# Optimization experiments

Measured on AMD Instinct MI355X. Metric: run time of the kernel, lower is better.

## Reference

```python
import jax, jax.numpy as jnp
import numpy as np

NUM_HEADS = 12


def get_rel_pos(q_size, k_size, rel_pos):
    # rel_pos: (2*max(q,k)-1, head_dim); sizes match table here so no resize.
    max_rel_dist = int(2 * max(q_size, k_size) - 1)
    if rel_pos.shape[0] != max_rel_dist:
        rel_pos = jax.image.resize(rel_pos, (max_rel_dist, rel_pos.shape[1]), method='linear')
    q_coords = jnp.arange(q_size)[:, None] * max(k_size / q_size, 1.0)
    k_coords = jnp.arange(k_size)[None, :] * max(q_size / k_size, 1.0)
    rel = (q_coords - k_coords + (k_size - 1) * max(q_size / k_size, 1.0)).astype(jnp.int32)
    return rel_pos[rel.reshape(-1)].reshape(q_size, k_size, -1)  # (q, k, head_dim)


def setup_inputs() -> dict:
    key = jax.random.key(0)
    ks = jax.random.split(key, 7)
    B, H, W, C = 8, 32, 32, 768
    head_dim = C // NUM_HEADS
    return {
        'x': jax.random.normal(ks[0], (B, H, W, C), jnp.float32),
        'w_qkv': jax.random.normal(ks[1], (C, 3 * C), jnp.float32) * 0.02,
        'b_qkv': jnp.zeros((3 * C,), jnp.float32),
        'rel_pos_h': jax.random.normal(ks[2], (2 * H - 1, head_dim), jnp.float32) * 0.02,
        'rel_pos_w': jax.random.normal(ks[3], (2 * W - 1, head_dim), jnp.float32) * 0.02,
        'w_proj': jax.random.normal(ks[4], (C, C), jnp.float32) * 0.02,
        'b_proj': jnp.zeros((C,), jnp.float32),
    }


def reference(x, w_qkv, b_qkv, rel_pos_h, rel_pos_w, w_proj, b_proj):
    B, H, W, C = x.shape
    heads = NUM_HEADS
    hd = C // heads
    S = H * W
    qkv = x @ w_qkv + b_qkv                                  # (B,H,W,3C)
    qkv = qkv.reshape(B, S, 3, heads, hd).transpose(2, 0, 3, 1, 4)
    qkv = qkv.reshape(3, B * heads, S, hd)
    q, k, v = qkv[0], qkv[1], qkv[2]
    attn = (q * hd ** -0.5) @ k.transpose(0, 2, 1)           # (B*heads, S, S)
    rh = get_rel_pos(H, H, rel_pos_h)                        # (H,H,hd)
    rw = get_rel_pos(W, W, rel_pos_w)                        # (W,W,hd)
    r_q = q.reshape(B * heads, H, W, hd)
    rel_h = jnp.einsum('bhwc,hkc->bhwk', r_q, rh)
    rel_w = jnp.einsum('bhwc,wkc->bhwk', r_q, rw)
    attn = (attn.reshape(B * heads, H, W, H, W)
            + rel_h[:, :, :, :, None]
            + rel_w[:, :, :, None, :]).reshape(B * heads, S, S)
    attn = jax.nn.softmax(attn, axis=-1)
    out = (attn @ v).reshape(B, heads, H, W, hd).transpose(0, 2, 3, 1, 4).reshape(B, H, W, C)
    return out @ w_proj + b_proj
```

## Files before the change

### kernel.cpp

```cpp
#include <hip/hip_runtime.h>
#include <hip/hip_bf16.h>

#define BATCH 8
#define SEQ   1024
#define CH    768
#define NH    12
#define HD    64
#define BH    96
#define N_QKV 2304

#define LOG2E 1.44269504088896f

typedef __attribute__((ext_vector_type(8))) short bfrag;
typedef __attribute__((ext_vector_type(4))) short short4v;
typedef __attribute__((ext_vector_type(4))) float ffrag;
typedef __attribute__((ext_vector_type(4))) int  intv4;
typedef __attribute__((ext_vector_type(2))) int  intv2;

__device__ __forceinline__ short f2bf(float x) {
    __hip_bfloat16 h = __float2bfloat16(x);
    return *reinterpret_cast<short*>(&h);
}
__device__ __forceinline__ float bf2f(short b) {
    __hip_bfloat16 h;
    *reinterpret_cast<short*>(&h) = b;
    return __bfloat162float(h);
}
__device__ __forceinline__ void split2(float x, short& hi, short& lo) {
    short h = f2bf(x);
    hi = h;
    lo = f2bf(x - bf2f(h));
}
__device__ __forceinline__ void async_copy16(void* lds, const void* g) {
    __builtin_amdgcn_global_load_lds(
        (const __attribute__((address_space(1))) void*)g,
        (__attribute__((address_space(3))) void*)lds, 16, 0, 0);
}
__device__ __forceinline__ void pinned_load16(intv4& dst, const void* p) {
    asm volatile("global_load_dwordx4 %0, %1, off"
                 : "=&v"(dst) : "v"((unsigned long long)p));
}

__global__ __launch_bounds__(256) void prep(
    const float* __restrict__ x,
    const float* __restrict__ w_qkv, const float* __restrict__ w_proj,
    short* __restrict__ Xh,
    short* __restrict__ WqhT,
    short* __restrict__ WphT, short* __restrict__ WplT)
{
    __shared__ float ts[32][33];
    const int tid = threadIdx.x;
    const int bid = blockIdx.x;

    if (bid < 512) {
        const int n4 = (BATCH * SEQ * CH) / 4;
        for (int i = bid * 256 + tid; i < n4; i += 512 * 256) {
            float4 f = ((const float4*)x)[i];
            short4v h;
            h[0] = f2bf(f.x); h[1] = f2bf(f.y); h[2] = f2bf(f.z); h[3] = f2bf(f.w);
            ((short4v*)Xh)[i] = h;
        }
        return;
    }
    if (bid < 2240) {
        int t = bid - 512;
        const int bx = t % 72, by = t / 72;
        const int r0 = by * 32, c0 = bx * 32;
        #pragma unroll
        for (int i = 0; i < 4; ++i) {
            int idx = tid + i * 256;
            int rr = idx >> 5, cc = idx & 31;
            ts[rr][cc] = w_qkv[(size_t)(r0 + rr) * N_QKV + c0 + cc];
        }
        __syncthreads();
        #pragma unroll
        for (int i = 0; i < 4; ++i) {
            int idx = tid + i * 256;
            int rr = idx >> 5, cc = idx & 31;
            WqhT[(size_t)(c0 + rr) * CH + r0 + cc] = f2bf(ts[cc][rr]);
        }
        return;
    }
    {
        int t = bid - 2240;
        const int bx = t % 24, by = t / 24;
        const int r0 = by * 32, c0 = bx * 32;
        #pragma unroll
        for (int i = 0; i < 4; ++i) {
            int idx = tid + i * 256;
            int rr = idx >> 5, cc = idx & 31;
            ts[rr][cc] = w_proj[(size_t)(r0 + rr) * CH + c0 + cc];
        }
        __syncthreads();
        #pragma unroll
        for (int i = 0; i < 4; ++i) {
            int idx = tid + i * 256;
            int rr = idx >> 5, cc = idx & 31;
            short h, l;
            split2(ts[cc][rr], h, l);
            WphT[(size_t)(c0 + rr) * CH + r0 + cc] = h;
            WplT[(size_t)(c0 + rr) * CH + r0 + cc] = l;
        }
    }
}

__device__ __forceinline__ void gemm_core1(
    short* lds,
    const short* __restrict__ Ah, const short* __restrict__ BhT,
    int m0, int n0, ffrag acc[4][4])
{
    const int tid = threadIdx.x;
    const int wave = tid >> 6, lane = tid & 63;
    const int quad = lane >> 4, l16 = lane & 15;
    const int wm = (wave & 1) * 64, wn = (wave >> 1) * 64;

    const int arr  = wave >> 1;
    const int half = wave & 1;
    const short* src = arr ? BhT : Ah;
    const int row0 = (arr ? n0 : m0) + half * 64;
    const size_t lane_off = (size_t)(lane >> 3) * CH + (size_t)((lane & 7) ^ (lane >> 3)) * 8;
    const short* sbase = src + (size_t)row0 * CH + lane_off;
    short* ldsw = lds + arr * 8192 + half * 4096;

    for (int c = 0; c < 12; ++c) {
        __syncthreads();
        #pragma unroll
        for (int i = 0; i < 8; ++i)
            async_copy16(ldsw + i * 512, sbase + (size_t)i * 8 * CH + c * 64);
        __syncthreads();

        #pragma unroll
        for (int kc = 0; kc < 2; ++kc) {
            bfrag ah[4], bh[4];
            const int xs = ((kc * 4 + quad) ^ (l16 & 7)) * 8;
            #pragma unroll
            for (int i = 0; i < 4; ++i) {
                ah[i] = *(const bfrag*)&lds[(wm + i * 16 + l16) * 64 + xs];
                bh[i] = *(const bfrag*)&lds[8192 + (wn + i * 16 + l16) * 64 + xs];
            }
            #pragma unroll
            for (int mi = 0; mi < 4; ++mi)
                #pragma unroll
                for (int ni = 0; ni < 4; ++ni)
                    acc[mi][ni] = __builtin_amdgcn_mfma_f32_16x16x32_bf16(ah[mi], bh[ni], acc[mi][ni], 0, 0, 0);
        }
    }
}

__device__ __forceinline__ void gemm_core3(
    short* lds,
    const short* __restrict__ Ah, const short* __restrict__ Al,
    const short* __restrict__ BhT, const short* __restrict__ BlT,
    int m0, int n0, ffrag acc[4][4])
{
    const int tid = threadIdx.x;
    const int wave = tid >> 6, lane = tid & 63;
    const int quad = lane >> 4, l16 = lane & 15;
    const int wm = (wave & 1) * 64, wn = (wave >> 1) * 64;

    const short* src;
    int row0;
    if (wave == 0)      { src = Ah;  row0 = m0; }
    else if (wave == 1) { src = Al;  row0 = m0; }
    else if (wave == 2) { src = BhT; row0 = n0; }
    else                { src = BlT; row0 = n0; }
    const size_t lane_off = (size_t)(lane >> 3) * CH + (size_t)((lane & 7) ^ (lane >> 3)) * 8;
    const short* sbase = src + (size_t)row0 * CH + lane_off;
    short* ldsw = lds + wave * 8192;

    for (int c = 0; c < 12; ++c) {
        __syncthreads();
        #pragma unroll
        for (int i = 0; i < 16; ++i)
            async_copy16(ldsw + i * 512, sbase + (size_t)i * 8 * CH + c * 64);
        __syncthreads();

        #pragma unroll
        for (int kc = 0; kc < 2; ++kc) {
            bfrag ah[4], al[4], bh[4], bl[4];
            const int xs = ((kc * 4 + quad) ^ (l16 & 7)) * 8;
            #pragma unroll
            for (int i = 0; i < 4; ++i) {
                int ra = (wm + i * 16 + l16) * 64 + xs;
                int rb = (wn + i * 16 + l16) * 64 + xs;
                ah[i] = *(const bfrag*)&lds[ra];
                al[i] = *(const bfrag*)&lds[8192 + ra];
                bh[i] = *(const bfrag*)&lds[16384 + rb];
                bl[i] = *(const bfrag*)&lds[24576 + rb];
            }
            #pragma unroll
            for (int mi = 0; mi < 4; ++mi)
                #pragma unroll
                for (int ni = 0; ni < 4; ++ni) {
                    acc[mi][ni] = __builtin_amdgcn_mfma_f32_16x16x32_bf16(ah[mi], bh[ni], acc[mi][ni], 0, 0, 0);
                    acc[mi][ni] = __builtin_amdgcn_mfma_f32_16x16x32_bf16(ah[mi], bl[ni], acc[mi][ni], 0, 0, 0);
                    acc[mi][ni] = __builtin_amdgcn_mfma_f32_16x16x32_bf16(al[mi], bh[ni], acc[mi][ni], 0, 0, 0);
                }
        }
    }
}

__global__ __launch_bounds__(256) void gemm_qkv_mfma(
    const short* __restrict__ Xh,
    const short* __restrict__ WhT,
    const float* __restrict__ bias,
    short* __restrict__ qh, short* __restrict__ kh, short* __restrict__ vT)
{
    __shared__ short lds[2 * 8192];
    const int id  = blockIdx.x;
    const int xcd = id & 7;
    const int per = id >> 3;
    const int mi_ = per & 7;
    const int ni_ = per >> 3;
    const int m0 = (xcd * 8 + mi_) * 128;
    const int n0 = ni_ * 128;
    const int which = n0 / CH;

    ffrag acc[4][4];
    #pragma unroll
    for (int i = 0; i < 4; ++i)
        #pragma unroll
        for (int j = 0; j < 4; ++j) acc[i][j] = (ffrag){0.f, 0.f, 0.f, 0.f};

    gemm_core1(lds, Xh, WhT, m0, n0, acc);

    const int tid = threadIdx.x;
    const int wave = tid >> 6, lane = tid & 63;
    const int quad = lane >> 4, l16 = lane & 15;
    const int wm = (wave & 1) * 64, wn = (wave >> 1) * 64;
    const int b = m0 >> 10;

    #pragma unroll
    for (int ni = 0; ni < 4; ++ni) {
        int n = n0 + wn + ni * 16 + l16;
        float bv = bias[n];
        int nin = n - which * CH;
        int head = nin >> 6, d = nin & 63;
        #pragma unroll
        for (int mi = 0; mi < 4; ++mi) {
            if (which == 2) {
                int s_base = (m0 & 1023) + wm + mi * 16 + quad * 4;
                short4v pk;
                #pragma unroll
                for (int r = 0; r < 4; ++r) pk[r] = f2bf(acc[mi][ni][r] + bv);
                *(short4v*)&vT[((size_t)(b * NH + head) * HD + d) * SEQ + s_base] = pk;
            } else {
                const float scale = (which == 0) ? 0.125f * LOG2E : 1.0f;
                short* dst = (which == 0) ? qh : kh;
                #pragma unroll
                for (int r = 0; r < 4; ++r) {
                    int m = m0 + wm + mi * 16 + quad * 4 + r;
                    int s = m & 1023;
                    dst[((size_t)(b * NH + head) * SEQ + s) * HD + d] =
                        f2bf((acc[mi][ni][r] + bv) * scale);
                }
            }
        }
    }
}

__global__ __launch_bounds__(256) void gemm_proj_mfma(
    const short* __restrict__ Ah, const short* __restrict__ Al,
    const short* __restrict__ WhT, const short* __restrict__ WlT,
    const float* __restrict__ bias, float* __restrict__ out)
{
    __shared__ short lds[4 * 8192];
    const int id  = blockIdx.x;
    const int xcd = id & 7;
    const int per = id >> 3;
    const int mi_ = per & 7;
    const int ni_ = per >> 3;
    const int m0 = (xcd * 8 + mi_) * 128;
    const int n0 = ni_ * 128;

    ffrag acc[4][4];
    #pragma unroll
    for (int i = 0; i < 4; ++i)
        #pragma unroll
        for (int j = 0; j < 4; ++j) acc[i][j] = (ffrag){0.f, 0.f, 0.f, 0.f};

    gemm_core3(lds, Ah, Al, WhT, WlT, m0, n0, acc);

    const int tid = threadIdx.x;
    const int wave = tid >> 6, lane = tid & 63;
    const int quad = lane >> 4, l16 = lane & 15;
    const int wm = (wave & 1) * 64, wn = (wave >> 1) * 64;

    #pragma unroll
    for (int ni = 0; ni < 4; ++ni) {
        int n = n0 + wn + ni * 16 + l16;
        float bv = bias[n];
        #pragma unroll
        for (int mi = 0; mi < 4; ++mi)
            #pragma unroll
            for (int r = 0; r < 4; ++r) {
                int m = m0 + wm + mi * 16 + quad * 4 + r;
                out[(size_t)m * CH + n] = acc[mi][ni][r] + bv;
            }
    }
}

__global__ __launch_bounds__(256, 3) void attn_kernel(
    const short* __restrict__ qh,
    const short* __restrict__ kh_g, const short* __restrict__ vT_g,
    const float* __restrict__ rph,
    const float* __restrict__ rpw,
    short* __restrict__ aoh, short* __restrict__ aol)
{
    const int fid   = blockIdx.x;
    const int xcd   = fid & 7;
    const int inner = fid >> 3;
    const int s0    = (inner & 7) * 128;
    const int bh    = xcd * 12 + (inner >> 3);

    const int tid  = threadIdx.x;
    const int wave = tid >> 6;
    const int lane = tid & 63;
    const int quad = lane >> 4;
    const int l16  = lane & 15;

    __shared__ short Kh[64 * 64];
    __shared__ short Vth[64 * 64];
    __shared__ short Th[128][68];
    __shared__ short Tw_Ps[128 * 68];

    const size_t bh_koff = (size_t)bh * SEQ * HD;
    const size_t bh_voff = (size_t)bh * HD * SEQ;
    const size_t klane = (size_t)(lane >> 3) * HD + (size_t)((lane & 7) ^ (lane >> 3)) * 8;

    const short* kbase = kh_g + bh_koff + klane;
    const int i0 = wave * 2;
    short* KhW0 = Kh + i0 * 512 + lane * 8;

    const short* vgbase = vT_g + bh_voff
        + (size_t)(wave * 16 + (lane >> 3)) * SEQ + (size_t)(lane & 7) * 8;

    int vwA[2], vwB[2];
    {
        const int m  = lane & 7;
        const int oA = ((m >> 2) << 2) + ((m & 1) << 1);
        const int hf = (m >> 1) & 1;
        #pragma unroll
        for (int jj = 0; jj < 2; ++jj) {
            int d = wave * 16 + jj * 8 + (lane >> 3);
            vwA[jj] = d * 64 + ((oA ^ (d & 7)) << 3) + hf * 4;
            vwB[jj] = d * 64 + (((oA + 1) ^ (d & 7)) << 3) + hf * 4;
        }
    }

    intv4 kA0, kA1, vA0, vA1, kB0, kB1, vB0, vB1;
    pinned_load16(kA0, kbase + (size_t)(i0 * 8) * HD);
    pinned_load16(kA1, kbase + (size_t)(i0 * 8 + 8) * HD);
    pinned_load16(vA0, vgbase);
    pinned_load16(vA1, vgbase + (size_t)8 * SEQ);

    bfrag qfh[2][2];
    #pragma unroll
    for (int g = 0; g < 2; ++g) {
        const size_t qrow = ((size_t)bh * SEQ + s0 + wave * 32 + g * 16 + l16) * HD;
        #pragma unroll
        for (int kc = 0; kc < 2; ++kc)
            qfh[g][kc] = *(const bfrag*)(qh + qrow + kc * 32 + quad * 8);
    }

    #pragma unroll
    for (int table = 0; table < 2; ++table) {
        const float* tbl = table ? rpw : rph;
        #pragma unroll
        for (int n0r = 0; n0r < 64; n0r += 16) {
            int r = n0r + l16;
            bfrag bfr[2];
            #pragma unroll
            for (int kc = 0; kc < 2; ++kc) {
                if (r < 63) {
                    const float* trow = tbl + (size_t)r * HD + kc * 32 + quad * 8;
                    float4 f0 = *(const float4*)(trow);
                    float4 f1 = *(const float4*)(trow + 4);
                    float xs[8] = {f0.x, f0.y, f0.z, f0.w, f1.x, f1.y, f1.z, f1.w};
                    #pragma unroll
                    for (int j = 0; j < 8; ++j) bfr[kc][j] = f2bf(xs[j]);
                } else {
                    #pragma unroll
                    for (int j = 0; j < 8; ++j) bfr[kc][j] = 0;
                }
            }
            #pragma unroll
            for (int g = 0; g < 2; ++g) {
                ffrag acc = {0.f, 0.f, 0.f, 0.f};
                acc = __builtin_amdgcn_mfma_f32_16x16x32_bf16(qfh[g][0], bfr[0], acc, 0, 0, 0);
                acc = __builtin_amdgcn_mfma_f32_16x16x32_bf16(qfh[g][1], bfr[1], acc, 0, 0, 0);
                int row = wave * 32 + g * 16 + quad * 4;
                #pragma unroll
                for (int reg = 0; reg < 4; ++reg) {
                    short v = f2bf(acc[reg] * 8.0f);
                    if (table) Tw_Ps[(row + reg) * 68 + n0r + l16] = v;
                    else       Th[row + reg][n0r + l16] = v;
                }
            }
        }
    }

    float tw_r[2][2][4];
    #pragma unroll
    for (int g = 0; g < 2; ++g) {
        int qloc = wave * 32 + g * 16 + l16;
        int wq = g * 16 + l16;
        #pragma unroll
        for (int p = 0; p < 2; ++p)
            #pragma unroll
            for (int reg = 0; reg < 4; ++reg)
                tw_r[g][p][reg] = bf2f(Tw_Ps[qloc * 68 + (wq - (p * 16 + quad * 4 + reg) + 31)]);
    }
    const int hq_w = (s0 >> 5) + wave;

    float l_part[2] = {0.f, 0.f};
    ffrag Ot[2][4];
    #pragma unroll
    for (int g = 0; g < 2; ++g)
        #pragma unroll
        for (int t = 0; t < 4; ++t) Ot[g][t] = (ffrag){0.f, 0.f, 0.f, 0.f};

    auto chunk = [&](int c, const intv4& ck0, const intv4& ck1,
                     const intv4& cv0, const intv4& cv1,
                     intv4& nk0, intv4& nk1, intv4& nv0, intv4& nv1) {
        __syncthreads();
        if (c < 15) {
            const int cn = c + 1;
            pinned_load16(nk0, kbase + (size_t)(cn * 64 + i0 * 8) * HD);
            pinned_load16(nk1, kbase + (size_t)(cn * 64 + i0 * 8 + 8) * HD);
            pinned_load16(nv0, vgbase + cn * 64);
            pinned_load16(nv1, vgbase + (size_t)8 * SEQ + cn * 64);
            asm volatile("s_waitcnt vmcnt(4)");
        } else {
            asm volatile("s_waitcnt vmcnt(0)");
        }
        __builtin_amdgcn_sched_barrier(0);
        *(intv4*)KhW0         = ck0;
        *(intv4*)(KhW0 + 512) = ck1;
        {
            intv2 lo0 = {cv0[0], cv0[1]}, hi0 = {cv0[2], cv0[3]};
            intv2 lo1 = {cv1[0], cv1[1]}, hi1 = {cv1[2], cv1[3]};
            *(intv2*)&Vth[vwA[0]] = lo0;
            *(intv2*)&Vth[vwB[0]] = hi0;
            *(intv2*)&Vth[vwA[1]] = lo1;
            *(intv2*)&Vth[vwB[1]] = hi1;
        }
        __syncthreads();

        float th_r[2][2];
        #pragma unroll
        for (int g = 0; g < 2; ++g) {
            int qloc = wave * 32 + g * 16 + l16;
            th_r[g][0] = bf2f(Th[qloc][hq_w - 2 * c + 31]);
            th_r[g][1] = bf2f(Th[qloc][hq_w - 2 * c - 1 + 31]);
        }

        #pragma unroll
        for (int ktp = 0; ktp < 2; ++ktp) {
            bfrag kbhE[2], kbhO[2];
            #pragma unroll
            for (int kc = 0; kc < 2; ++kc) {
                int xs = ((kc * 4 + quad) ^ (l16 & 7)) * 8;
                kbhE[kc] = *(const bfrag*)&Kh[((2 * ktp) * 16 + l16) * 64 + xs];
                kbhO[kc] = *(const bfrag*)&Kh[((2 * ktp + 1) * 16 + l16) * 64 + xs];
            }
            bfrag pf[2];
            #pragma unroll
            for (int g = 0; g < 2; ++g) {
                ffrag aE, aO;
                #pragma unroll
                for (int reg = 0; reg < 4; ++reg) {
                    aE[reg] = th_r[g][ktp] + tw_r[g][0][reg];
                    aO[reg] = th_r[g][ktp] + tw_r[g][1][reg];
                }
                __builtin_amdgcn_s_setprio(1);
                aE = __builtin_amdgcn_mfma_f32_16x16x32_bf16(kbhE[0], qfh[g][0], aE, 0, 0, 0);
                aE = __builtin_amdgcn_mfma_f32_16x16x32_bf16(kbhE[1], qfh[g][1], aE, 0, 0, 0);
                aO = __builtin_amdgcn_mfma_f32_16x16x32_bf16(kbhO[0], qfh[g][0], aO, 0, 0, 0);
                aO = __builtin_amdgcn_mfma_f32_16x16x32_bf16(kbhO[1], qfh[g][1], aO, 0, 0, 0);
                __builtin_amdgcn_s_setprio(0);
                #pragma unroll
                for (int reg = 0; reg < 4; ++reg) {
                    float pE = exp2f(aE[reg]);
                    float pO = exp2f(aO[reg]);
                    l_part[g] += pE + pO;
                    pf[g][reg]     = f2bf(pE);
                    pf[g][reg + 4] = f2bf(pO);
                }
            }
            #pragma unroll
            for (int t = 0; t < 4; ++t) {
                int d = t * 16 + l16;
                int xv = ((ktp * 4 + quad) ^ (l16 & 7)) * 8;
                bfrag vh = *(const bfrag*)&Vth[d * 64 + xv];
                __builtin_amdgcn_s_setprio(1);
                #pragma unroll
                for (int g = 0; g < 2; ++g)
                    Ot[g][t] = __builtin_amdgcn_mfma_f32_16x16x32_bf16(pf[g], vh, Ot[g][t], 0, 0, 0);
                __builtin_amdgcn_s_setprio(0);
            }
        }
    };

    for (int cc = 0; cc < 8; ++cc) {
        chunk(2 * cc,     kA0, kA1, vA0, vA1, kB0, kB1, vB0, vB1);
        chunk(2 * cc + 1, kB0, kB1, vB0, vB1, kA0, kA1, vA0, vA1);
    }

    {
        int b = bh / NH, head = bh % NH;
        #pragma unroll
        for (int g = 0; g < 2; ++g) {
            float r = l_part[g];
            r += __shfl_xor(r, 16, 64);
            r += __shfl_xor(r, 32, 64);
            float invl = 1.f / r;
            float inv[4];
            #pragma unroll
            for (int reg = 0; reg < 4; ++reg)
                inv[reg] = __shfl(invl, quad * 4 + reg, 16);
            #pragma unroll
            for (int t = 0; t < 4; ++t) {
                #pragma unroll
                for (int reg = 0; reg < 4; ++reg) {
                    int s_ = s0 + wave * 32 + g * 16 + quad * 4 + reg;
                    int d = t * 16 + l16;
                    size_t idx = ((size_t)(b * SEQ + s_)) * CH + head * HD + d;
                    short h, l;
                    split2(Ot[g][t][reg] * inv[reg], h, l);
                    aoh[idx] = h;
                    aol[idx] = l;
                }
            }
        }
    }
}

extern "C" void kernel_launch(void* const* d_in, const int* in_sizes, int n_in,
                              void* d_out, int out_size, void* d_ws, size_t ws_size,
                              hipStream_t stream) {
    const float* x       = (const float*)d_in[0];
    const float* w_qkv   = (const float*)d_in[1];
    const float* b_qkv   = (const float*)d_in[2];
    const float* rph     = (const float*)d_in[3];
    const float* rpw     = (const float*)d_in[4];
    const float* w_proj  = (const float*)d_in[5];
    const float* b_proj  = (const float*)d_in[6];
    float* out = (float*)d_out;

    const size_t NTOK = (size_t)BATCH * SEQ;
    const size_t XSZ  = NTOK * CH;
    const size_t WQSZ = (size_t)N_QKV * CH;
    const size_t WPSZ = (size_t)CH * CH;
    short* Xh   = (short*)d_ws;
    short* AoL  = Xh + XSZ;
    short* WqhT = AoL + XSZ;
    short* WphT = WqhT + WQSZ;
    short* WplT = WphT + WPSZ;
    short* qh = WplT + WPSZ;
    short* kh = qh + XSZ;
    short* vT = kh + XSZ;
    short* aoh = Xh;
    short* aol = AoL;

    prep<<<dim3(2816), 256, 0, stream>>>(x, w_qkv, w_proj,
                                         Xh, WqhT, WphT, WplT);
    gemm_qkv_mfma<<<dim3(1152), 256, 0, stream>>>(Xh, WqhT, b_qkv,
                                                  qh, kh, vT);
    attn_kernel<<<dim3(768), 256, 0, stream>>>(qh, kh, vT,
                                               rph, rpw, aoh, aol);
    gemm_proj_mfma<<<dim3(384), 256, 0, stream>>>(aoh, aol, WphT, WplT,
                                                  b_proj, out);
}
```

Before: 226.0 us.

## Double-buffer LDS in QKV and projection GEMM cores with K-chunk prefetch

Result: no change. 227.2 us (+0.6%).

```diff
diff --git a/kernel.cpp b/kernel.cpp
--- a/kernel.cpp
+++ b/kernel.cpp
@@ -118,32 +118,48 @@
     const int half = wave & 1;
     const short* src = arr ? BhT : Ah;
     const int row0 = (arr ? n0 : m0) + half * 64;
-    const size_t lane_off = (size_t)(lane >> 3) * CH + (size_t)((lane & 7) ^ (lane >> 3)) * 8;
+    const size_t lane_off = (size_t)(lane >> 2) * CH
+                          + (size_t)((lane & 3) ^ ((lane >> 3) & 3)) * 8;
     const short* sbase = src + (size_t)row0 * CH + lane_off;
-    short* ldsw = lds + arr * 8192 + half * 4096;
-
-    for (int c = 0; c < 12; ++c) {
-        __syncthreads();
-        #pragma unroll
-        for (int i = 0; i < 8; ++i)
-            async_copy16(ldsw + i * 512, sbase + (size_t)i * 8 * CH + c * 64);
-        __syncthreads();
-
-        #pragma unroll
-        for (int kc = 0; kc < 2; ++kc) {
-            bfrag ah[4], bh[4];
-            const int xs = ((kc * 4 + quad) ^ (l16 & 7)) * 8;
-            #pragma unroll
-            for (int i = 0; i < 4; ++i) {
-                ah[i] = *(const bfrag*)&lds[(wm + i * 16 + l16) * 64 + xs];
-                bh[i] = *(const bfrag*)&lds[8192 + (wn + i * 16 + l16) * 64 + xs];
-            }
-            #pragma unroll
-            for (int mi = 0; mi < 4; ++mi)
-                #pragma unroll
-                for (int ni = 0; ni < 4; ++ni)
-                    acc[mi][ni] = __builtin_amdgcn_mfma_f32_16x16x32_bf16(ah[mi], bh[ni], acc[mi][ni], 0, 0, 0);
-        }
+    short* wsec = lds + arr * 4096 + half * 2048;
+
+    const int xs = (quad ^ ((l16 >> 1) & 3)) * 8;
+
+    #pragma unroll
+    for (int i = 0; i < 4; ++i)
+        async_copy16(wsec + i * 512, sbase + (size_t)i * 16 * CH);
+
+    for (int c = 0; c < 24; ++c) {
+        const int cur = c & 1;
+        if (c < 23) {
+            short* w = wsec + (cur ^ 1) * 8192;
+            #pragma unroll
+            for (int i = 0; i < 4; ++i)
+                async_copy16(w + i * 512,
+                             sbase + (size_t)i * 16 * CH + (c + 1) * 32);
+            asm volatile("s_waitcnt vmcnt(4)");
+        } else {
+            asm volatile("s_waitcnt vmcnt(0)");
+        }
+        __builtin_amdgcn_s_barrier();
+        __builtin_amdgcn_sched_barrier(0);
+
+        const short* Ab = lds + cur * 8192;
+        const short* Bb = Ab + 4096;
+        bfrag ah[4], bh[4];
+        #pragma unroll
+        for (int i = 0; i < 4; ++i) {
+            ah[i] = *(const bfrag*)&Ab[(wm + i * 16 + l16) * 32 + xs];
+            bh[i] = *(const bfrag*)&Bb[(wn + i * 16 + l16) * 32 + xs];
+        }
+        #pragma unroll
+        for (int mi = 0; mi < 4; ++mi)
+            #pragma unroll
+            for (int ni = 0; ni < 4; ++ni)
+                acc[mi][ni] = __builtin_amdgcn_mfma_f32_16x16x32_bf16(
+                    ah[mi], bh[ni], acc[mi][ni], 0, 0, 0);
+
+        __builtin_amdgcn_s_barrier();
     }
 }
 
@@ -164,39 +180,53 @@
     else if (wave == 1) { src = Al;  row0 = m0; }
     else if (wave == 2) { src = BhT; row0 = n0; }
     else                { src = BlT; row0 = n0; }
-    const size_t lane_off = (size_t)(lane >> 3) * CH + (size_t)((lane & 7) ^ (lane >> 3)) * 8;
+    const size_t lane_off = (size_t)(lane >> 2) * CH
+                          + (size_t)((lane & 3) ^ ((lane >> 3) & 3)) * 8;
     const short* sbase = src + (size_t)row0 * CH + lane_off;
-    short* ldsw = lds + wave * 8192;
-
-    for (int c = 0; c < 12; ++c) {
-        __syncthreads();
-        #pragma unroll
-        for (int i = 0; i < 16; ++i)
-            async_copy16(ldsw + i * 512, sbase + (size_t)i * 8 * CH + c * 64);
-        __syncthreads();
-
-        #pragma unroll
-        for (int kc = 0; kc < 2; ++kc) {
-            bfrag ah[4], al[4], bh[4], bl[4];
-            const int xs = ((kc * 4 + quad) ^ (l16 & 7)) * 8;
-            #pragma unroll
-            for (int i = 0; i < 4; ++i) {
-                int ra = (wm + i * 16 + l16) * 64 + xs;
-                int rb = (wn + i * 16 + l16) * 64 + xs;
-                ah[i] = *(const bfrag*)&lds[ra];
-                al[i] = *(const bfrag*)&lds[8192 + ra];
-                bh[i] = *(const bfrag*)&lds[16384 + rb];
-                bl[i] = *(const bfrag*)&lds[24576 + rb];
-            }
-            #pragma unroll
-            for (int mi = 0; mi < 4; ++mi)
-                #pragma unroll
-                for (int ni = 0; ni < 4; ++ni) {
-                    acc[mi][ni] = __builtin_amdgcn_mfma_f32_16x16x32_bf16(ah[mi], bh[ni], acc[mi][ni], 0, 0, 0);
-                    acc[mi][ni] = __builtin_amdgcn_mfma_f32_16x16x32_bf16(ah[mi], bl[ni], acc[mi][ni], 0, 0, 0);
-                    acc[mi][ni] = __builtin_amdgcn_mfma_f32_16x16x32_bf16(al[mi], bh[ni], acc[mi][ni], 0, 0, 0);
-                }
-        }
+    short* wsec = lds + wave * 4096;
+
+    const int xs = (quad ^ ((l16 >> 1) & 3)) * 8;
+
+    #pragma unroll
+    for (int i = 0; i < 8; ++i)
+        async_copy16(wsec + i * 512, sbase + (size_t)i * 16 * CH);
+
+    for (int c = 0; c < 24; ++c) {
+        const int cur = c & 1;
+        if (c < 23) {
+            short* w = wsec + (cur ^ 1) * 16384;
+            #pragma unroll
+            for (int i = 0; i < 8; ++i)
+                async_copy16(w + i * 512,
+                             sbase + (size_t)i * 16 * CH + (c + 1) * 32);
+            asm volatile("s_waitcnt vmcnt(8)");
+        } else {
+            asm volatile("s_waitcnt vmcnt(0)");
+        }
+        __builtin_amdgcn_s_barrier();
+        __builtin_amdgcn_sched_barrier(0);
+
+        const short* base = lds + cur * 16384;
+        bfrag ah[4], al[4], bh[4], bl[4];
+        #pragma unroll
+        for (int i = 0; i < 4; ++i) {
+            int ra = (wm + i * 16 + l16) * 32 + xs;
+            int rb = (wn + i * 16 + l16) * 32 + xs;
+            ah[i] = *(const bfrag*)&base[ra];
+            al[i] = *(const bfrag*)&base[4096 + ra];
+            bh[i] = *(const bfrag*)&base[8192 + rb];
+            bl[i] = *(const bfrag*)&base[12288 + rb];
+        }
+        #pragma unroll
+        for (int mi = 0; mi < 4; ++mi)
+            #pragma unroll
+            for (int ni = 0; ni < 4; ++ni) {
+                acc[mi][ni] = __builtin_amdgcn_mfma_f32_16x16x32_bf16(ah[mi], bh[ni], acc[mi][ni], 0, 0, 0);
+                acc[mi][ni] = __builtin_amdgcn_mfma_f32_16x16x32_bf16(ah[mi], bl[ni], acc[mi][ni], 0, 0, 0);
+                acc[mi][ni] = __builtin_amdgcn_mfma_f32_16x16x32_bf16(al[mi], bh[ni], acc[mi][ni], 0, 0, 0);
+            }
+
+        __builtin_amdgcn_s_barrier();
     }
 }
 
@@ -264,7 +294,7 @@
     const short* __restrict__ WhT, const short* __restrict__ WlT,
     const float* __restrict__ bias, float* __restrict__ out)
 {
-    __shared__ short lds[4 * 8192];
+    __shared__ short lds[2 * 16384];
     const int id  = blockIdx.x;
     const int xcd = id & 7;
     const int per = id >> 3;
```
